# Kernel tuning notes

Measured on AMD Instinct MI355X. Metric: run time of the kernel, lower is better.

## Reference

```python
import jax, jax.numpy as jnp
import numpy as np

B, L, NS, EPS = 512, 20, 16, 32   # sessions, seq_len, nodes/session, edges/session
H, V, STEP = 128, 100000, 1       # hidden, vocab (n_node), ggnn layers


def _xavier(key, shape):
    fan_out, fan_in = shape[0], shape[1]
    a = float(np.sqrt(6.0 / (fan_in + fan_out)))
    return jax.random.uniform(key, shape, minval=-a, maxval=a, dtype=jnp.float32)


def setup_inputs() -> dict:
    key = jax.random.key(0)
    ks = jax.random.split(key, 20)
    # node item ids per session (nonzero)
    items = jax.random.randint(ks[0], (B, NS), 1, V)
    # intra-session edges, offset to global node indices
    src_l = jax.random.randint(ks[1], (B, EPS), 0, NS)
    dst_l = jax.random.randint(ks[2], (B, EPS), 0, NS)
    offs = (jnp.arange(B) * NS)[:, None]
    edge_index = jnp.stack([(src_l + offs).reshape(-1), (dst_l + offs).reshape(-1)])
    # sequences drawn from each session's own nodes, padded with 0
    seq_pos = jax.random.randint(ks[3], (B, L), 0, NS)
    lengths = jax.random.randint(ks[4], (B,), 5, L + 1)
    mask = (jnp.arange(L)[None, :] < lengths[:, None]).astype(jnp.int32)
    sequence = jnp.where(mask == 1, jnp.take_along_axis(items, seq_pos, axis=1), 0)

    stdv = 1.0 / float(np.sqrt(H))
    embedding = jax.random.uniform(ks[5], (V, H), minval=-stdv, maxval=stdv, dtype=jnp.float32)
    embedding = embedding.at[0].set(0.0)  # padding_idx=0
    ggnn_w = _xavier(ks[6], (STEP * H, H)).reshape(STEP, H, H)
    W_ih = _xavier(ks[7], (3 * H, H))
    W_hh = _xavier(ks[8], (3 * H, H))
    b_ih = jnp.zeros((3 * H,), jnp.float32)
    b_hh = jnp.zeros((3 * H,), jnp.float32)
    W1 = _xavier(ks[9], (H, H)); b1 = jnp.zeros((H,), jnp.float32)
    W2 = _xavier(ks[10], (H, H)); b2 = jnp.zeros((H,), jnp.float32)
    w3 = _xavier(ks[11], (1, H))
    Wt = _xavier(ks[12], (H, 2 * H)); bt = jnp.zeros((H,), jnp.float32)
    gamma = jnp.ones((H,), jnp.float32); beta = jnp.zeros((H,), jnp.float32)
    return dict(items=items, edge_index=edge_index, sequence=sequence, mask=mask,
                embedding=embedding, ggnn_w=ggnn_w, W_ih=W_ih, W_hh=W_hh,
                b_ih=b_ih, b_hh=b_hh, W1=W1, b1=b1, W2=W2, b2=b2, w3=w3,
                Wt=Wt, bt=bt, gamma=gamma, beta=beta)


def reference(items, edge_index, sequence, mask, embedding, ggnn_w, W_ih, W_hh,
              b_ih, b_hh, W1, b1, W2, b2, w3, Wt, bt, gamma, beta):
    N = B * NS
    x = embedding[items.reshape(-1)]               # [N, H] node features
    src, dst = edge_index[0], edge_index[1]
    # GatedGraphConv: per-layer linear, scatter-add aggregation, GRUCell update
    for l in range(STEP):
        m = x @ ggnn_w[l]                          # [N, H]
        agg = jax.ops.segment_sum(m[src], dst, num_segments=N)
        gi = agg @ W_ih.T + b_ih                   # [N, 3H]
        gh = x @ W_hh.T + b_hh
        ir, iz, inn = jnp.split(gi, 3, axis=-1)
        hr, hz, hn = jnp.split(gh, 3, axis=-1)
        r = jax.nn.sigmoid(ir + hr)
        z = jax.nn.sigmoid(iz + hz)
        n = jnp.tanh(inn + r * hn)
        x = (1.0 - z) * n + z * x
    xg = x.reshape(B, NS, H)
    # ragged gather: for each seq position, first node whose item id matches
    match = sequence[:, :, None] == items[:, None, :]      # [B, L, NS]
    has = match.any(-1)
    idx = jnp.argmax(match, axis=-1)                       # first match
    gathered = jnp.take_along_axis(xg, idx[..., None], axis=1)  # [B, L, H]
    fallback = embedding[sequence]                         # item not in graph
    hidden = jnp.where(has[..., None], gathered, fallback)
    hidden = jnp.where((sequence == 0)[..., None], 0.0, hidden)
    # compute_scores: attention pooling + hybrid transform + layernorm
    seq_lens = mask.sum(axis=1) - 1
    ht = hidden[jnp.arange(B), seq_lens]                   # [B, H] last item
    q1 = (ht @ W1.T + b1)[:, None, :]                      # [B, 1, H]
    q2 = hidden @ W2.T + b2                                # [B, L, H]
    alpha = jax.nn.sigmoid(q1 + q2) @ w3.T                 # [B, L, 1]
    mf = mask[..., None].astype(hidden.dtype)
    a = jnp.sum(alpha * hidden * mf, axis=1)               # [B, H]
    a = jnp.concatenate([a, ht], axis=1) @ Wt.T + bt       # hybrid (nonhybrid=False)
    mu = a.mean(-1, keepdims=True)
    var = ((a - mu) ** 2).mean(-1, keepdims=True)
    a = (a - mu) / jnp.sqrt(var + 1e-5) * gamma + beta
    scores = a @ embedding[1:].T                           # [B, V-1]
    return scores
```

## Files before the change

kernel.cpp:

```cpp
#include <hip/hip_runtime.h>
#include <hip/hip_bf16.h>
#include <hip/hip_fp16.h>

#define B_ 512
#define L_ 20
#define NS_ 16
#define EPS_ 32
#define H_ 128
#define V_ 100000
#define N_NODES (B_*NS_)
#define N_EDGES (B_*EPS_)
#define NV (V_-1)

typedef _Float16 half8 __attribute__((ext_vector_type(8)));
typedef float floatx4 __attribute__((ext_vector_type(4)));

#define PITCH 136

__global__ void k_prep(const int* __restrict__ items, const float* __restrict__ emb,
                       const float* __restrict__ Wg, const float* __restrict__ Whh,
                       const float* __restrict__ Wih, const float* __restrict__ W2,
                       const float* __restrict__ W1,
                       float* __restrict__ x, _Float16* __restrict__ WgT_h,
                       _Float16* __restrict__ Whh_h, _Float16* __restrict__ Wih_h,
                       _Float16* __restrict__ W2_h, _Float16* __restrict__ W1_h) {
  int i = blockIdx.x*256 + threadIdx.x;
  if (i < N_NODES*H_) {
    int n = i >> 7, h = i & 127;
    x[i] = emb[(size_t)items[n]*H_ + h];
    return;
  }
  i -= N_NODES*H_;
  if (i < H_*H_) { int j = i>>7, k = i&127; WgT_h[i] = (_Float16)Wg[k*H_ + j]; return; }
  i -= H_*H_;
  if (i < 3*H_*H_) { Whh_h[i] = (_Float16)Whh[i]; return; }
  i -= 3*H_*H_;
  if (i < 3*H_*H_) { Wih_h[i] = (_Float16)Wih[i]; return; }
  i -= 3*H_*H_;
  if (i < H_*H_) { W2_h[i] = (_Float16)W2[i]; return; }
  i -= H_*H_;
  if (i < H_*H_) { W1_h[i] = (_Float16)W1[i]; return; }
}

__global__ __launch_bounds__(256) void k_gemm128(
    const float* __restrict__ A, const _Float16* __restrict__ B0,
    const _Float16* __restrict__ B1, int switch_mt,
    float* __restrict__ C, int N) {
  __shared__ _Float16 lds_a[64*PITCH];
  __shared__ _Float16 lds_b[64*PITCH];
  const int tid = threadIdx.x;
  const int mt = blockIdx.y, nt = blockIdx.x;
  const _Float16* __restrict__ Bp = (mt < switch_mt) ? B0 : B1;
  #pragma unroll
  for (int i = 0; i < 8; i++) {
    int lin = i*256 + tid;
    int row = lin >> 5, c4 = lin & 31;
    const float4 v = *reinterpret_cast<const float4*>(&A[(size_t)(mt*64+row)*H_ + c4*4]);
    union { _Float16 h[4]; uint2 u; } p;
    p.h[0]=(_Float16)v.x; p.h[1]=(_Float16)v.y; p.h[2]=(_Float16)v.z; p.h[3]=(_Float16)v.w;
    *reinterpret_cast<uint2*>(&lds_a[row*PITCH + c4*4]) = p.u;
  }
  #pragma unroll
  for (int i = 0; i < 4; i++) {
    int lin = i*256 + tid;
    int row = lin >> 4, ch = lin & 15;
    uint4 v = *reinterpret_cast<const uint4*>(&Bp[(size_t)(nt*64+row)*H_ + ch*8]);
    *reinterpret_cast<uint4*>(&lds_b[row*PITCH + ch*8]) = v;
  }
  __syncthreads();
  const int w = tid >> 6, lane = tid & 63, quad = lane >> 4, r16 = lane & 15;
  half8 afr[4];
  #pragma unroll
  for (int kk = 0; kk < 4; kk++)
    afr[kk] = *reinterpret_cast<const half8*>(&lds_a[(w*16 + r16)*PITCH + kk*32 + quad*8]);
  floatx4 acc[4];
  #pragma unroll
  for (int n4 = 0; n4 < 4; n4++) acc[n4] = (floatx4){0.f,0.f,0.f,0.f};
  #pragma unroll
  for (int n4 = 0; n4 < 4; n4++) {
    #pragma unroll
    for (int kk = 0; kk < 4; kk++) {
      half8 bfr = *reinterpret_cast<const half8*>(&lds_b[(n4*16 + r16)*PITCH + kk*32 + quad*8]);
      acc[n4] = __builtin_amdgcn_mfma_f32_16x16x32_f16(afr[kk], bfr, acc[n4], 0, 0, 0);
    }
  }
  #pragma unroll
  for (int n4 = 0; n4 < 4; n4++)
    #pragma unroll
    for (int r = 0; r < 4; r++) {
      int row = mt*64 + w*16 + quad*4 + r;
      int col = nt*64 + n4*16 + r16;
      C[(size_t)row*N + col] = acc[n4][r];
    }
}

#define GILP 385
__global__ __launch_bounds__(256) void k_gnn(
    const int* __restrict__ edge_index, const float* __restrict__ mgh,
    const _Float16* __restrict__ Wih, const float* __restrict__ b_ih,
    const float* __restrict__ b_hh, float* __restrict__ x) {
  __shared__ __align__(16) _Float16 a16[NS_*PITCH];
  __shared__ __align__(16) float gil[NS_*GILP];
  float* agg = gil;
  const int b = blockIdx.x, tid = threadIdx.x;
  if (tid < 128) {
    #pragma unroll
    for (int j = 0; j < NS_; j++) agg[j*128 + tid] = 0.f;
    for (int e = 0; e < EPS_; e++) {
      int se = edge_index[b*EPS_ + e];
      int de = edge_index[N_EDGES + b*EPS_ + e] - b*NS_;
      agg[de*128 + tid] += mgh[(size_t)se*512 + tid];
    }
  }
  __syncthreads();
  #pragma unroll
  for (int j = 0; j < 8; j++) {
    int idx = j*256 + tid;
    a16[(idx >> 7)*PITCH + (idx & 127)] = (_Float16)agg[idx];
  }
  __syncthreads();
  const int w = tid >> 6, lane = tid & 63, quad = lane >> 4, r16 = lane & 15;
  half8 afr[4];
  #pragma unroll
  for (int kk = 0; kk < 4; kk++)
    afr[kk] = *reinterpret_cast<const half8*>(&a16[r16*PITCH + kk*32 + quad*8]);
  floatx4 acc[6];
  #pragma unroll
  for (int t = 0; t < 6; t++) acc[t] = (floatx4){0.f,0.f,0.f,0.f};
  #pragma unroll
  for (int t = 0; t < 6; t++) {
    int g = w*6 + t;
    #pragma unroll
    for (int kk = 0; kk < 4; kk++) {
      half8 bfr = *reinterpret_cast<const half8*>(&Wih[(size_t)(g*16 + r16)*H_ + kk*32 + quad*8]);
      acc[t] = __builtin_amdgcn_mfma_f32_16x16x32_f16(afr[kk], bfr, acc[t], 0, 0, 0);
    }
  }
  #pragma unroll
  for (int t = 0; t < 6; t++)
    #pragma unroll
    for (int r = 0; r < 4; r++)
      gil[(quad*4 + r)*GILP + (w*6 + t)*16 + r16] = acc[t][r];
  __syncthreads();
  #pragma unroll
  for (int j = 0; j < 8; j++) {
    int idx = j*256 + tid;
    int nl = idx >> 7, h = idx & 127;
    size_t node = (size_t)b*NS_ + nl;
    float ir  = gil[nl*GILP + h]       + b_ih[h];
    float iz  = gil[nl*GILP + 128 + h] + b_ih[128 + h];
    float in_ = gil[nl*GILP + 256 + h] + b_ih[256 + h];
    float hr  = mgh[node*512 + 128 + h] + b_hh[h];
    float hz  = mgh[node*512 + 256 + h] + b_hh[128 + h];
    float hn  = mgh[node*512 + 384 + h] + b_hh[256 + h];
    float rr = 1.f/(1.f + __expf(-(ir + hr)));
    float zz = 1.f/(1.f + __expf(-(iz + hz)));
    float nn = tanhf(in_ + rr*hn);
    x[node*H_ + h] = (1.f - zz)*nn + zz*x[node*H_ + h];
  }
}

__global__ void k_hidden(const int* __restrict__ items, const int* __restrict__ sequence,
                         const int* __restrict__ mask, const float* __restrict__ xg,
                         const float* __restrict__ emb, float* __restrict__ Hbuf) {
  int tid = threadIdx.x;
  int r = blockIdx.x*2 + (tid >> 7);
  int h = tid & 127;
  int b, l;
  if (r < B_*L_) { b = r / L_; l = r - b*L_; }
  else {
    b = r - B_*L_;
    int len = 0;
    for (int i = 0; i < L_; i++) len += mask[b*L_ + i];
    l = len - 1;
  }
  int seqv = sequence[b*L_ + l];
  float val = 0.f;
  if (seqv != 0) {
    int idx = -1;
    #pragma unroll
    for (int j = 0; j < NS_; j++) { if (idx < 0 && items[b*NS_ + j] == seqv) idx = j; }
    val = (idx >= 0) ? xg[(size_t)(b*NS_ + idx)*H_ + h] : emb[(size_t)seqv*H_ + h];
  }
  Hbuf[(size_t)r*H_ + h] = val;
}

__global__ __launch_bounds__(128) void k_attn(
    const float* __restrict__ Hbuf, const float* __restrict__ q,
    const float* __restrict__ b1, const float* __restrict__ b2,
    const float* __restrict__ w3, const float* __restrict__ Wt,
    const float* __restrict__ bt, const float* __restrict__ gamma,
    const float* __restrict__ beta, _Float16* __restrict__ a_h) {
  __shared__ float red[2];
  __shared__ float cat[256];
  const int b = blockIdx.x, t = threadIdx.x;
  float q1b = q[(size_t)(B_*L_ + b)*H_ + t] + b1[t] + b2[t];
  float w3t = w3[t];
  float at = 0.f;
  for (int l = 0; l < L_; l++) {
    float s = q1b + q[(size_t)(b*L_ + l)*H_ + t];
    float v = (1.f/(1.f + __expf(-s))) * w3t;
    #pragma unroll
    for (int o = 32; o > 0; o >>= 1) v += __shfl_down(v, o);
    if ((t & 63) == 0) red[t >> 6] = v;
    __syncthreads();
    float alpha = red[0] + red[1];
    __syncthreads();
    at += alpha * Hbuf[(size_t)(b*L_ + l)*H_ + t];
  }
  float htv = Hbuf[(size_t)(B_*L_ + b)*H_ + t];
  cat[t] = at; cat[128 + t] = htv;
  __syncthreads();
  float hyb = bt[t];
  const float* wrow = &Wt[(size_t)t*256];
  #pragma unroll 4
  for (int k = 0; k < 256; k++) hyb += cat[k]*wrow[k];
  float s = hyb;
  #pragma unroll
  for (int o = 32; o > 0; o >>= 1) s += __shfl_down(s, o);
  if ((t & 63) == 0) red[t >> 6] = s;
  __syncthreads();
  float mu = (red[0] + red[1]) * (1.f/128.f);
  __syncthreads();
  float d = hyb - mu;
  float s2 = d*d;
  #pragma unroll
  for (int o = 32; o > 0; o >>= 1) s2 += __shfl_down(s2, o);
  if ((t & 63) == 0) red[t >> 6] = s2;
  __syncthreads();
  float var = (red[0] + red[1]) * (1.f/128.f);
  float y = d * rsqrtf(var + 1e-5f) * gamma[t] + beta[t];
  a_h[(size_t)b*H_ + t] = (_Float16)y;
}

__global__ __launch_bounds__(256) void k_scores(
    const _Float16* __restrict__ a_h, const float* __restrict__ emb,
    float* __restrict__ out) {
  __shared__ _Float16 lds_a[128*PITCH];
  __shared__ _Float16 lds_b[64*PITCH];
  const int tid = threadIdx.x;
  const int d = blockIdx.x;
  const int nt = (d >> 5)*8 + (d & 7);
  const int mg = (d >> 3) & 3;
  if (nt >= 1563) return;
  #pragma unroll
  for (int i = 0; i < 8; i++) {
    int lin = i*256 + tid;
    int row = lin >> 4, ch = lin & 15;
    uint4 v = *reinterpret_cast<const uint4*>(&a_h[(size_t)(mg*128 + row)*H_ + ch*8]);
    *reinterpret_cast<uint4*>(&lds_a[row*PITCH + ch*8]) = v;
  }
  #pragma unroll
  for (int i = 0; i < 8; i++) {
    int lin = i*256 + tid;
    int row = lin >> 5, c4 = lin & 31;
    int g = nt*64 + row;
    float4 v = {0.f, 0.f, 0.f, 0.f};
    if (g < NV) v = *reinterpret_cast<const float4*>(&emb[(size_t)(1 + g)*H_ + c4*4]);
    union { _Float16 h[4]; uint2 u; } p;
    p.h[0]=(_Float16)v.x; p.h[1]=(_Float16)v.y; p.h[2]=(_Float16)v.z; p.h[3]=(_Float16)v.w;
    *reinterpret_cast<uint2*>(&lds_b[row*PITCH + c4*4]) = p.u;
  }
  __syncthreads();
  const int w = tid >> 6, lane = tid & 63, quad = lane >> 4, r16 = lane & 15;
  half8 afr[2][4];
  #pragma unroll
  for (int ms = 0; ms < 2; ms++)
    #pragma unroll
    for (int kk = 0; kk < 4; kk++)
      afr[ms][kk] = *reinterpret_cast<const half8*>(&lds_a[(w*32 + ms*16 + r16)*PITCH + kk*32 + quad*8]);
  floatx4 acc[2][4];
  #pragma unroll
  for (int ms = 0; ms < 2; ms++)
    #pragma unroll
    for (int n4 = 0; n4 < 4; n4++) acc[ms][n4] = (floatx4){0.f,0.f,0.f,0.f};
  #pragma unroll
  for (int n4 = 0; n4 < 4; n4++) {
    #pragma unroll
    for (int kk = 0; kk < 4; kk++) {
      half8 bfr = *reinterpret_cast<const half8*>(&lds_b[(n4*16 + r16)*PITCH + kk*32 + quad*8]);
      acc[0][n4] = __builtin_amdgcn_mfma_f32_16x16x32_f16(afr[0][kk], bfr, acc[0][n4], 0, 0, 0);
      acc[1][n4] = __builtin_amdgcn_mfma_f32_16x16x32_f16(afr[1][kk], bfr, acc[1][n4], 0, 0, 0);
    }
  }
  #pragma unroll
  for (int ms = 0; ms < 2; ms++)
    #pragma unroll
    for (int n4 = 0; n4 < 4; n4++)
      #pragma unroll
      for (int r = 0; r < 4; r++) {
        int row = mg*128 + w*32 + ms*16 + quad*4 + r;
        int col = nt*64 + n4*16 + r16;
        if (col < NV) out[(size_t)row*NV + col] = acc[ms][n4][r];
      }
}

extern "C" void kernel_launch(void* const* d_in, const int* in_sizes, int n_in,
                              void* d_out, int out_size, void* d_ws, size_t ws_size,
                              hipStream_t stream) {
  const int*   items     = (const int*)d_in[0];
  const int*   edge_index= (const int*)d_in[1];
  const int*   sequence  = (const int*)d_in[2];
  const int*   mask      = (const int*)d_in[3];
  const float* emb       = (const float*)d_in[4];
  const float* ggnn_w    = (const float*)d_in[5];
  const float* W_ih      = (const float*)d_in[6];
  const float* W_hh      = (const float*)d_in[7];
  const float* b_ih      = (const float*)d_in[8];
  const float* b_hh      = (const float*)d_in[9];
  const float* W1        = (const float*)d_in[10];
  const float* b1        = (const float*)d_in[11];
  const float* W2        = (const float*)d_in[12];
  const float* b2        = (const float*)d_in[13];
  const float* w3        = (const float*)d_in[14];
  const float* Wt        = (const float*)d_in[15];
  const float* bt        = (const float*)d_in[16];
  const float* gamma     = (const float*)d_in[17];
  const float* beta      = (const float*)d_in[18];

  char* ws = (char*)d_ws;
  float* x    = (float*)(ws + 0);
  float* mgh  = (float*)(ws + 4194304);
  float* q    = (float*)(ws + 4194304);
  float* Hbuf = (float*)(ws + 20971520);
  _Float16* a_h   = (_Float16*)(ws + 39059456);
  _Float16* WgT_h = (_Float16*)(ws + 39190528);
  _Float16* Whh_h = (_Float16*)(ws + 39223296);
  _Float16* Wih_h = (_Float16*)(ws + 39321600);
  _Float16* W2_h  = (_Float16*)(ws + 39419904);
  _Float16* W1_h  = (_Float16*)(ws + 39452672);
  float* out = (float*)d_out;

  k_prep<<<4672, 256, 0, stream>>>(items, emb, ggnn_w, W_hh, W_ih, W2, W1,
                                   x, WgT_h, Whh_h, Wih_h, W2_h, W1_h);
  k_gemm128<<<dim3(8, 128), 256, 0, stream>>>(x, WgT_h, WgT_h, 1 << 30, mgh, 512);
  k_gnn<<<512, 256, 0, stream>>>(edge_index, mgh, Wih_h, b_ih, b_hh, x);
  k_hidden<<<5376, 256, 0, stream>>>(items, sequence, mask, x, emb, Hbuf);
  k_gemm128<<<dim3(2, 168), 256, 0, stream>>>(Hbuf, W2_h, W1_h, 160, q, 128);
  k_attn<<<512, 128, 0, stream>>>(Hbuf, q, b1, b2, w3, Wt, bt, gamma, beta, a_h);
  k_scores<<<6272, 256, 0, stream>>>(a_h, emb, out);
}
```

Measured before the change: 449.4 us.

## Fuse hidden gather, query GEMMs and attention into one per-session kernel

Replaces the three kernels for hidden gather, the W1/W2 query GEMM and attention/layernorm with a single per-session block. That block gathers the hidden rows into shared memory, computes q2 with MFMA and q1 with a dot product, then does the attention pooling, hybrid transform and layernorm locally. This removes two launches and the global round trips for Hbuf and q. The score kernel also drops its swizzled 1D block mapping in favour of a plain 2D grid, which may change L2 reuse of the embedding tiles.

New measurement: 408.6 us. 1.1x faster.

```diff
diff --git a/kernel.cpp b/kernel.cpp
--- a/kernel.cpp
+++ b/kernel.cpp
@@ -160,77 +160,139 @@
   }
 }
 
-__global__ void k_hidden(const int* __restrict__ items, const int* __restrict__ sequence,
-                         const int* __restrict__ mask, const float* __restrict__ xg,
-                         const float* __restrict__ emb, float* __restrict__ Hbuf) {
-  int tid = threadIdx.x;
-  int r = blockIdx.x*2 + (tid >> 7);
-  int h = tid & 127;
-  int b, l;
-  if (r < B_*L_) { b = r / L_; l = r - b*L_; }
-  else {
-    b = r - B_*L_;
-    int len = 0;
-    for (int i = 0; i < L_; i++) len += mask[b*L_ + i];
-    l = len - 1;
-  }
-  int seqv = sequence[b*L_ + l];
-  float val = 0.f;
-  if (seqv != 0) {
-    int idx = -1;
-    #pragma unroll
-    for (int j = 0; j < NS_; j++) { if (idx < 0 && items[b*NS_ + j] == seqv) idx = j; }
-    val = (idx >= 0) ? xg[(size_t)(b*NS_ + idx)*H_ + h] : emb[(size_t)seqv*H_ + h];
-  }
-  Hbuf[(size_t)r*H_ + h] = val;
-}
-
-__global__ __launch_bounds__(128) void k_attn(
-    const float* __restrict__ Hbuf, const float* __restrict__ q,
+__global__ __launch_bounds__(256) void k_sess(
+    const int* __restrict__ items, const int* __restrict__ sequence,
+    const int* __restrict__ mask, const float* __restrict__ xg,
+    const float* __restrict__ emb,
+    const _Float16* __restrict__ W2h, const _Float16* __restrict__ W1h,
     const float* __restrict__ b1, const float* __restrict__ b2,
     const float* __restrict__ w3, const float* __restrict__ Wt,
     const float* __restrict__ bt, const float* __restrict__ gamma,
     const float* __restrict__ beta, _Float16* __restrict__ a_h) {
-  __shared__ float red[2];
+  __shared__ float hid[21*H_];
+  __shared__ __align__(16) _Float16 a16[32*PITCH];
+  __shared__ float qs[20*H_];
+  __shared__ float q1full[H_];
+  __shared__ float alphas[20];
   __shared__ float cat[256];
-  const int b = blockIdx.x, t = threadIdx.x;
-  float q1b = q[(size_t)(B_*L_ + b)*H_ + t] + b1[t] + b2[t];
-  float w3t = w3[t];
-  float at = 0.f;
-  for (int l = 0; l < L_; l++) {
-    float s = q1b + q[(size_t)(b*L_ + l)*H_ + t];
-    float v = (1.f/(1.f + __expf(-s))) * w3t;
+  __shared__ float red4[4];
+  const int b = blockIdx.x, tid = threadIdx.x;
+  int len = 0;
+  #pragma unroll
+  for (int i = 0; i < L_; i++) len += mask[b*L_ + i];
+  #pragma unroll
+  for (int j = 0; j < 10; j++) {
+    int r = j*2 + (tid >> 7);
+    int h = tid & 127;
+    int seqv = sequence[b*L_ + r];
+    float val = 0.f;
+    if (seqv != 0) {
+      int idx = -1;
+      #pragma unroll
+      for (int jj = 0; jj < NS_; jj++) { if (idx < 0 && items[b*NS_ + jj] == seqv) idx = jj; }
+      val = (idx >= 0) ? xg[(size_t)(b*NS_ + idx)*H_ + h] : emb[(size_t)seqv*H_ + h];
+    }
+    hid[r*H_ + h] = val;
+    a16[r*PITCH + h] = (_Float16)val;
+  }
+  #pragma unroll
+  for (int j = 0; j < 6; j++) {
+    int idx = j*256 + tid;
+    a16[(20 + (idx >> 7))*PITCH + (idx & 127)] = (_Float16)0.f;
+  }
+  __syncthreads();
+  if (tid < 128) hid[20*H_ + tid] = hid[(len-1)*H_ + tid];
+  __syncthreads();
+  const int w = tid >> 6, lane = tid & 63, quad = lane >> 4, r16 = lane & 15;
+  {
+    half8 afr[2][4];
+    #pragma unroll
+    for (int mt = 0; mt < 2; mt++)
+      #pragma unroll
+      for (int kk = 0; kk < 4; kk++)
+        afr[mt][kk] = *reinterpret_cast<const half8*>(&a16[(mt*16 + r16)*PITCH + kk*32 + quad*8]);
+    floatx4 acc[2][2];
+    #pragma unroll
+    for (int mt = 0; mt < 2; mt++)
+      #pragma unroll
+      for (int nt = 0; nt < 2; nt++) acc[mt][nt] = (floatx4){0.f,0.f,0.f,0.f};
+    #pragma unroll
+    for (int nt = 0; nt < 2; nt++) {
+      #pragma unroll
+      for (int kk = 0; kk < 4; kk++) {
+        half8 bfr = *reinterpret_cast<const half8*>(&W2h[(size_t)((w*2 + nt)*16 + r16)*H_ + kk*32 + quad*8]);
+        acc[0][nt] = __builtin_amdgcn_mfma_f32_16x16x32_f16(afr[0][kk], bfr, acc[0][nt], 0, 0, 0);
+        acc[1][nt] = __builtin_amdgcn_mfma_f32_16x16x32_f16(afr[1][kk], bfr, acc[1][nt], 0, 0, 0);
+      }
+    }
+    #pragma unroll
+    for (int mt = 0; mt < 2; mt++)
+      #pragma unroll
+      for (int nt = 0; nt < 2; nt++)
+        #pragma unroll
+        for (int r = 0; r < 4; r++) {
+          int row = mt*16 + quad*4 + r;
+          if (row < 20) qs[row*H_ + (w*2 + nt)*16 + r16] = acc[mt][nt][r];
+        }
+  }
+  if (tid < 128) {
+    float s = b1[tid] + b2[tid];
+    const half8* wrow = reinterpret_cast<const half8*>(&W1h[(size_t)tid*H_]);
+    #pragma unroll
+    for (int k8 = 0; k8 < 16; k8++) {
+      half8 hv = wrow[k8];
+      #pragma unroll
+      for (int u = 0; u < 8; u++) s += hid[20*H_ + k8*8 + u] * (float)hv[u];
+    }
+    q1full[tid] = s;
+  }
+  __syncthreads();
+  for (int j = 0; j < 5; j++) {
+    int l = w*5 + j;
+    float v = 0.f;
+    #pragma unroll
+    for (int p = 0; p < 2; p++) {
+      int t = lane + p*64;
+      float s = q1full[t] + qs[l*H_ + t];
+      v += (1.f/(1.f + __expf(-s))) * w3[t];
+    }
     #pragma unroll
     for (int o = 32; o > 0; o >>= 1) v += __shfl_down(v, o);
-    if ((t & 63) == 0) red[t >> 6] = v;
-    __syncthreads();
-    float alpha = red[0] + red[1];
-    __syncthreads();
-    at += alpha * Hbuf[(size_t)(b*L_ + l)*H_ + t];
-  }
-  float htv = Hbuf[(size_t)(B_*L_ + b)*H_ + t];
-  cat[t] = at; cat[128 + t] = htv;
-  __syncthreads();
-  float hyb = bt[t];
-  const float* wrow = &Wt[(size_t)t*256];
-  #pragma unroll 4
-  for (int k = 0; k < 256; k++) hyb += cat[k]*wrow[k];
-  float s = hyb;
-  #pragma unroll
-  for (int o = 32; o > 0; o >>= 1) s += __shfl_down(s, o);
-  if ((t & 63) == 0) red[t >> 6] = s;
-  __syncthreads();
-  float mu = (red[0] + red[1]) * (1.f/128.f);
-  __syncthreads();
-  float d = hyb - mu;
+    if (lane == 0) alphas[l] = v;
+  }
+  __syncthreads();
+  if (tid < 128) {
+    float af = 0.f;
+    #pragma unroll
+    for (int l = 0; l < L_; l++) af += alphas[l]*hid[l*H_ + tid];
+    cat[tid] = af; cat[128 + tid] = hid[20*H_ + tid];
+  }
+  __syncthreads();
+  float hyb = 0.f;
+  if (tid < 128) {
+    hyb = bt[tid];
+    const float* wrow = &Wt[(size_t)tid*256];
+    #pragma unroll 4
+    for (int k = 0; k < 256; k++) hyb += cat[k]*wrow[k];
+  }
+  float s1 = (tid < 128) ? hyb : 0.f;
+  #pragma unroll
+  for (int o = 32; o > 0; o >>= 1) s1 += __shfl_down(s1, o);
+  if (lane == 0) red4[w] = s1;
+  __syncthreads();
+  float mu = (red4[0] + red4[1] + red4[2] + red4[3]) * (1.f/128.f);
+  __syncthreads();
+  float d = (tid < 128) ? (hyb - mu) : 0.f;
   float s2 = d*d;
   #pragma unroll
   for (int o = 32; o > 0; o >>= 1) s2 += __shfl_down(s2, o);
-  if ((t & 63) == 0) red[t >> 6] = s2;
-  __syncthreads();
-  float var = (red[0] + red[1]) * (1.f/128.f);
-  float y = d * rsqrtf(var + 1e-5f) * gamma[t] + beta[t];
-  a_h[(size_t)b*H_ + t] = (_Float16)y;
+  if (lane == 0) red4[w] = s2;
+  __syncthreads();
+  if (tid < 128) {
+    float var = (red4[0] + red4[1] + red4[2] + red4[3]) * (1.f/128.f);
+    float y = d * rsqrtf(var + 1e-5f) * gamma[tid] + beta[tid];
+    a_h[(size_t)b*H_ + tid] = (_Float16)y;
+  }
 }
 
 __global__ __launch_bounds__(256) void k_scores(
@@ -239,10 +301,7 @@
   __shared__ _Float16 lds_a[128*PITCH];
   __shared__ _Float16 lds_b[64*PITCH];
   const int tid = threadIdx.x;
-  const int d = blockIdx.x;
-  const int nt = (d >> 5)*8 + (d & 7);
-  const int mg = (d >> 3) & 3;
-  if (nt >= 1563) return;
+  const int nt = blockIdx.x, mg = blockIdx.y;
   #pragma unroll
   for (int i = 0; i < 8; i++) {
     int lin = i*256 + tid;
@@ -321,8 +380,6 @@
   char* ws = (char*)d_ws;
   float* x    = (float*)(ws + 0);
   float* mgh  = (float*)(ws + 4194304);
-  float* q    = (float*)(ws + 4194304);
-  float* Hbuf = (float*)(ws + 20971520);
   _Float16* a_h   = (_Float16*)(ws + 39059456);
   _Float16* WgT_h = (_Float16*)(ws + 39190528);
   _Float16* Whh_h = (_Float16*)(ws + 39223296);
@@ -335,8 +392,7 @@
                                    x, WgT_h, Whh_h, Wih_h, W2_h, W1_h);
   k_gemm128<<<dim3(8, 128), 256, 0, stream>>>(x, WgT_h, WgT_h, 1 << 30, mgh, 512);
   k_gnn<<<512, 256, 0, stream>>>(edge_index, mgh, Wih_h, b_ih, b_hh, x);
-  k_hidden<<<5376, 256, 0, stream>>>(items, sequence, mask, x, emb, Hbuf);
-  k_gemm128<<<dim3(2, 168), 256, 0, stream>>>(Hbuf, W2_h, W1_h, 160, q, 128);
-  k_attn<<<512, 128, 0, stream>>>(Hbuf, q, b1, b2, w3, Wt, bt, gamma, beta, a_h);
-  k_scores<<<6272, 256, 0, stream>>>(a_h, emb, out);
-}
+  k_sess<<<512, 256, 0, stream>>>(items, sequence, mask, x, emb, W2_h, W1_h,
+                                  b1, b2, w3, Wt, bt, gamma, beta, a_h);
+  k_scores<<<dim3(1563, 4), 256, 0, stream>>>(a_h, emb, out);
+}
```
